# Kernel optimization log

Measured on AMD Instinct MI355X. Metric: run time of the kernel, lower is better.

Reference implementation:

```python
import jax, jax.numpy as jnp
import numpy as np

IN_F = 4096
OUT_F = 4096
N_TOK = 8192
MAX_ITER = IN_F * OUT_F // 2  # default max_iter=-1 -> half of weight entries


def _approx_matmul(x, weight, max_iter):
    """Budgeted approximate matmul: only the `max_iter` largest-magnitude
    weight entries participate (the rest of the multiply-accumulate budget is
    skipped). Faithful to the iteration-budget semantics of Approx_Matmul:
    max_iter multiply-adds out of in_features*out_features total.
    """
    n = weight.size
    flat_abs = jnp.abs(weight).reshape(-1)
    # threshold = k-th largest magnitude (static k -> jit-friendly)
    kth = jnp.sort(flat_abs)[n - max_iter]
    mask = (jnp.abs(weight) >= kth).astype(weight.dtype)
    w_eff = weight * jax.lax.stop_gradient(mask)
    # y[t, o] = sum_i x[t, i] * w_eff[o, i]
    return jnp.einsum('ti,oi->to', x, w_eff)


def setup_inputs() -> dict:
    key = jax.random.key(0)
    kx, kw, kb = jax.random.split(key, 3)
    x = jax.random.normal(kx, (N_TOK, IN_F), dtype=jnp.float32)
    # kaiming_uniform_(a=sqrt(5)) on [out, in] -> bound = 1/sqrt(in_features)
    bound = 1.0 / np.sqrt(IN_F)
    weight = jax.random.uniform(kw, (OUT_F, IN_F), dtype=jnp.float32,
                                minval=-bound, maxval=bound)
    bias = jax.random.uniform(kb, (OUT_F,), dtype=jnp.float32,
                              minval=-bound, maxval=bound)
    return {"x": x, "weight": weight, "bias": bias}


def reference(x, weight, bias):
    mid = _approx_matmul(x, weight, MAX_ITER)
    return mid + bias
```

## Files before the change

kernel.cpp:

```cpp
#include <hip/hip_runtime.h>

#define IN_F   4096
#define OUT_F  4096
#define N_TOK  8192
#define NW     (OUT_F * IN_F)
#define SEL_TARGET 8388608u
#define CAND_CAP (1u << 20)

#define LO_BITS 0x3BFCA000u
#define HI_BITS 0x3C018000u

typedef unsigned int  u32;
typedef unsigned short u16;

typedef __bf16 bf16x8 __attribute__((ext_vector_type(8)));
typedef float  f32x4  __attribute__((ext_vector_type(4)));

__device__ inline u16 f2bf_rne(float f) {
    u32 u = __float_as_uint(f);
    u32 r = (u + 0x7fffu + ((u >> 16) & 1u)) >> 16;
    return (u16)r;
}

__global__ __launch_bounds__(256) void scan1_kernel(const uint4* __restrict__ wb,
                                                    u32* __restrict__ cand,
                                                    u32* __restrict__ scal) {
    __shared__ u32 lbuf[4096];
    __shared__ u32 lcnt, gbase, lblw;
    if (threadIdx.x == 0) { lcnt = 0; lblw = 0; }
    __syncthreads();

    const int base = blockIdx.x * 4096;
    u32 cntb = 0;
    #pragma unroll 4
    for (int j = 0; j < 16; j++) {
        uint4 v = wb[base + threadIdx.x + j * 256];
        u32 k[4] = {v.x & 0x7fffffffu, v.y & 0x7fffffffu,
                    v.z & 0x7fffffffu, v.w & 0x7fffffffu};
        #pragma unroll
        for (int e = 0; e < 4; e++) {
            u32 kk = k[e];
            cntb += (kk < LO_BITS) ? 1u : 0u;
            if (kk >= LO_BITS && kk < HI_BITS) {
                u32 idx = atomicAdd(&lcnt, 1u);
                if (idx < 4096) lbuf[idx] = kk;
                else scal[6] = 1u;
            }
        }
    }
    #pragma unroll
    for (int off = 32; off; off >>= 1) cntb += __shfl_down(cntb, off);
    if ((threadIdx.x & 63) == 0) atomicAdd(&lblw, cntb);
    __syncthreads();
    if (threadIdx.x == 0) {
        gbase = atomicAdd(&scal[3], min(lcnt, 4096u));
        atomicAdd(&scal[4], lblw);
    }
    __syncthreads();
    const u32 n = min(lcnt, 4096u), gb = gbase;
    for (u32 i = threadIdx.x; i < n; i += 256)
        if (gb + i < CAND_CAP) cand[gb + i] = lbuf[i];
}

#define SCAN1024(part, t)                                            \
    do { _Pragma("unroll")                                           \
        for (int off_ = 1; off_ < 1024; off_ <<= 1) {                \
            u32 v_ = ((t) >= off_) ? part[(t) - off_] : 0u;          \
            __syncthreads();                                         \
            part[t] += v_;                                           \
            __syncthreads();                                         \
        } } while (0)

__global__ __launch_bounds__(1024) void select_win_kernel(const u32* __restrict__ cand,
                                                          const uint4* __restrict__ wb,
                                                          u32* __restrict__ scal) {
    __shared__ u32 h[2048];
    __shared__ u32 part[1024];
    __shared__ u32 sh[2];
    const int t = threadIdx.x;
    const u32 n = scal[3], below = scal[4], ovf = scal[6];
    const bool valid = (n > 0) && (n <= CAND_CAP) && (ovf == 0) &&
                       (below <= SEL_TARGET) && (SEL_TARGET < below + n);

    if (valid) {
        u32 tgt = SEL_TARGET - below;
        const uint4* c4 = (const uint4*)cand;
        const u32 n4 = n >> 2;

        h[t] = 0; h[t + 1024] = 0;
        __syncthreads();
        for (u32 i = t; i < n4; i += 1024) {
            uint4 v = c4[i];
            atomicAdd(&h[(v.x - LO_BITS) >> 9], 1u);
            atomicAdd(&h[(v.y - LO_BITS) >> 9], 1u);
            atomicAdd(&h[(v.z - LO_BITS) >> 9], 1u);
            atomicAdd(&h[(v.w - LO_BITS) >> 9], 1u);
        }
        for (u32 i = (n4 << 2) + t; i < n; i += 1024)
            atomicAdd(&h[(cand[i] - LO_BITS) >> 9], 1u);
        __syncthreads();
        u32 c = h[t];
        part[t] = c;
        __syncthreads();
        SCAN1024(part, t);
        u32 cum = (t == 0) ? 0u : part[t - 1];
        if (tgt >= cum && tgt < cum + c) { sh[0] = (u32)t; sh[1] = tgt - cum; }
        __syncthreads();
        const u32 b1 = sh[0];
        tgt = sh[1];
        __syncthreads();

        h[t] = 0; h[t + 1024] = 0;
        __syncthreads();
        for (u32 i = t; i < n4; i += 1024) {
            uint4 v = c4[i];
            u32 d0 = v.x - LO_BITS, d1 = v.y - LO_BITS,
                d2 = v.z - LO_BITS, d3 = v.w - LO_BITS;
            if ((d0 >> 9) == b1) atomicAdd(&h[d0 & 511u], 1u);
            if ((d1 >> 9) == b1) atomicAdd(&h[d1 & 511u], 1u);
            if ((d2 >> 9) == b1) atomicAdd(&h[d2 & 511u], 1u);
            if ((d3 >> 9) == b1) atomicAdd(&h[d3 & 511u], 1u);
        }
        for (u32 i = (n4 << 2) + t; i < n; i += 1024) {
            u32 d = cand[i] - LO_BITS;
            if ((d >> 9) == b1) atomicAdd(&h[d & 511u], 1u);
        }
        __syncthreads();
        c = (t < 512) ? h[t] : 0u;
        part[t] = c;
        __syncthreads();
        SCAN1024(part, t);
        cum = (t == 0) ? 0u : part[t - 1];
        if (tgt >= cum && tgt < cum + c)
            scal[2] = LO_BITS + (b1 << 9) + (u32)t;
        return;
    }

    u32 tgt = SEL_TARGET;
    const int nvec = NW / 4;
    h[t] = 0; h[t + 1024] = 0;
    __syncthreads();
    for (int i = t; i < nvec; i += 1024) {
        uint4 v = wb[i];
        atomicAdd(&h[(v.x & 0x7fffffffu) >> 20], 1u);
        atomicAdd(&h[(v.y & 0x7fffffffu) >> 20], 1u);
        atomicAdd(&h[(v.z & 0x7fffffffu) >> 20], 1u);
        atomicAdd(&h[(v.w & 0x7fffffffu) >> 20], 1u);
    }
    __syncthreads();
    u32 a0 = h[2 * t], a1 = h[2 * t + 1];
    part[t] = a0 + a1;
    __syncthreads();
    SCAN1024(part, t);
    u32 cum = (t == 0) ? 0u : part[t - 1];
    if (tgt >= cum && tgt < cum + a0) { sh[0] = (u32)(2 * t);     sh[1] = tgt - cum; }
    cum += a0;
    if (tgt >= cum && tgt < cum + a1) { sh[0] = (u32)(2 * t + 1); sh[1] = tgt - cum; }
    __syncthreads();
    const u32 b1f = sh[0];
    tgt = sh[1];
    __syncthreads();

    h[t] = 0; h[t + 1024] = 0;
    __syncthreads();
    for (int i = t; i < nvec; i += 1024) {
        uint4 v = wb[i];
        u32 k[4] = {v.x & 0x7fffffffu, v.y & 0x7fffffffu,
                    v.z & 0x7fffffffu, v.w & 0x7fffffffu};
        #pragma unroll
        for (int e = 0; e < 4; e++)
            if ((k[e] >> 20) == b1f) atomicAdd(&h[(k[e] >> 9) & 2047u], 1u);
    }
    __syncthreads();
    a0 = h[2 * t]; a1 = h[2 * t + 1];
    part[t] = a0 + a1;
    __syncthreads();
    SCAN1024(part, t);
    cum = (t == 0) ? 0u : part[t - 1];
    if (tgt >= cum && tgt < cum + a0) { sh[0] = (u32)(2 * t);     sh[1] = tgt - cum; }
    cum += a0;
    if (tgt >= cum && tgt < cum + a1) { sh[0] = (u32)(2 * t + 1); sh[1] = tgt - cum; }
    __syncthreads();
    const u32 pfx22 = (b1f << 11) | sh[0];
    tgt = sh[1];
    __syncthreads();

    h[t] = 0; h[t + 1024] = 0;
    __syncthreads();
    for (int i = t; i < nvec; i += 1024) {
        uint4 v = wb[i];
        u32 k[4] = {v.x & 0x7fffffffu, v.y & 0x7fffffffu,
                    v.z & 0x7fffffffu, v.w & 0x7fffffffu};
        #pragma unroll
        for (int e = 0; e < 4; e++)
            if ((k[e] >> 9) == pfx22) atomicAdd(&h[k[e] & 511u], 1u);
    }
    __syncthreads();
    u32 c = (t < 512) ? h[t] : 0u;
    part[t] = c;
    __syncthreads();
    SCAN1024(part, t);
    cum = (t == 0) ? 0u : part[t - 1];
    if (tgt >= cum && tgt < cum + c)
        scal[2] = (pfx22 << 9) | (u32)t;
}

__global__ __launch_bounds__(256) void convert_fused_kernel(
    const uint4* __restrict__ wb, const float4* __restrict__ xb,
    u16* __restrict__ w16, u16* __restrict__ x16,
    const u32* __restrict__ scal) {
    if (blockIdx.x < 1024) {
        const u32 kth = scal[2];
        const int stride = 1024 * 256;
        for (int i = blockIdx.x * 256 + threadIdx.x; i < NW / 4; i += stride) {
            uint4 v = wb[i];
            ushort4 o;
            o.x = ((v.x & 0x7fffffffu) >= kth) ? f2bf_rne(__uint_as_float(v.x)) : (u16)0;
            o.y = ((v.y & 0x7fffffffu) >= kth) ? f2bf_rne(__uint_as_float(v.y)) : (u16)0;
            o.z = ((v.z & 0x7fffffffu) >= kth) ? f2bf_rne(__uint_as_float(v.z)) : (u16)0;
            o.w = ((v.w & 0x7fffffffu) >= kth) ? f2bf_rne(__uint_as_float(v.w)) : (u16)0;
            *(ushort4*)&w16[(size_t)i * 4] = o;
        }
    } else {
        const int stride = 2048 * 256;
        for (int i = (blockIdx.x - 1024) * 256 + threadIdx.x;
             i < (N_TOK * IN_F) / 4; i += stride) {
            float4 v = xb[i];
            ushort4 o;
            o.x = f2bf_rne(v.x);
            o.y = f2bf_rne(v.y);
            o.z = f2bf_rne(v.z);
            o.w = f2bf_rne(v.w);
            *(ushort4*)&x16[(size_t)i * 4] = o;
        }
    }
}

#define BK 64
#define NT (IN_F / BK)

#define ASLOT(buf, ks) (((buf) * 2 + (ks)) * 8192)
#define BSLOT(buf, ks) (32768 + ((buf) * 2 + (ks)) * 8192)

#define VMCNT(n) asm volatile("s_waitcnt vmcnt(" #n ")" ::: "memory")
#define LGKM0    asm volatile("s_waitcnt lgkmcnt(0)" ::: "memory")
#define BARR()   __builtin_amdgcn_s_barrier()

__global__ __launch_bounds__(512, 2) void gemm8p(
    const u16* __restrict__ A,
    const u16* __restrict__ B,
    const float* __restrict__ bias,
    float* __restrict__ C) {
    __shared__ u16 lds[65536];

    const int tid  = threadIdx.x;
    const int lane = tid & 63;
    const int ln15 = lane & 15;
    const int l16  = lane >> 4;
    const int wv   = tid >> 6;
    const int wr   = wv >> 2;
    const int wc   = wv & 3;
    const int wrow = wr * 128;
    const int wcol = wc * 64;

    const int bid = blockIdx.x;
    const int swz = (bid & 7) * 64 + (bid >> 3);
    const int by  = swz >> 4;
    const int bx  = swz & 15;
    const int arow = by * 256;
    const int brow = bx * 256;

    f32x4 acc[8][4];
    #pragma unroll
    for (int m = 0; m < 8; m++)
        #pragma unroll
        for (int n = 0; n < 4; n++)
            acc[m][n] = {0.f, 0.f, 0.f, 0.f};

    #define STAGE(G, rowbase, kt, ks, slot) do {                                        \
        _Pragma("unroll")                                                               \
        for (int i_ = 0; i_ < 2; i_++) {                                                \
            int q_  = tid + i_ * 512;                                                   \
            int r_  = q_ >> 2;                                                          \
            int cs_ = (q_ & 3) ^ ((r_ >> 1) & 3);                                       \
            const u16* src_ = (G) + (size_t)((rowbase) + r_) * IN_F                     \
                              + (kt) * BK + (ks) * 32 + cs_ * 8;                        \
            __builtin_amdgcn_global_load_lds(                                           \
                (const __attribute__((address_space(1))) unsigned int*)src_,            \
                (__attribute__((address_space(3))) unsigned int*)&lds[(slot) + q_ * 8], \
                16, 0, 0);                                                              \
        } } while (0)

    #define READ_A(mh, ks, buf) do {                                                    \
        _Pragma("unroll")                                                               \
        for (int i_ = 0; i_ < 4; i_++) {                                                \
            int row_ = wrow + ((mh) * 4 + i_) * 16 + ln15;                              \
            int cc_  = l16 ^ ((row_ >> 1) & 3);                                         \
            aF[i_] = *(const bf16x8*)&lds[ASLOT(buf, ks) + row_ * 32 + cc_ * 8];        \
        } } while (0)

    #define READ_B(ks, buf) do {                                                       \
        _Pragma("unroll")                                                               \
        for (int i_ = 0; i_ < 4; i_++) {                                                \
            int row_ = wcol + i_ * 16 + ln15;                                           \
            int cc_  = l16 ^ ((row_ >> 1) & 3);                                         \
            bF[i_] = *(const bf16x8*)&lds[BSLOT(buf, ks) + row_ * 32 + cc_ * 8];        \
        } } while (0)

    #define MFMAQ(mh) do {                                                              \
        __builtin_amdgcn_s_setprio(1);                                                  \
        _Pragma("unroll")                                                               \
        for (int i_ = 0; i_ < 4; i_++)                                                  \
            _Pragma("unroll")                                                           \
            for (int n_ = 0; n_ < 4; n_++)                                              \
                acc[(mh) * 4 + i_][n_] = __builtin_amdgcn_mfma_f32_16x16x32_bf16(       \
                    aF[i_], bF[n_], acc[(mh) * 4 + i_][n_], 0, 0, 0);                   \
        __builtin_amdgcn_s_setprio(0);                                                  \
    } while (0)

    STAGE(B, brow, 0, 0, BSLOT(0, 0));
    STAGE(A, arow, 0, 0, ASLOT(0, 0));
    STAGE(B, brow, 0, 1, BSLOT(0, 1));
    STAGE(A, arow, 0, 1, ASLOT(0, 1));
    VMCNT(4);
    STAGE(B, brow, 1, 0, BSLOT(1, 0));
    STAGE(A, arow, 1, 0, ASLOT(1, 0));
    STAGE(B, brow, 1, 1, BSLOT(1, 1));
    VMCNT(6);
    BARR();

    bf16x8 aF[4], bF[4];

    #pragma unroll 1
    for (int it = 0; it < NT / 2; it++) {
        const int t0 = 2 * it;
        const int ka = t0 + 1;
        const int kb = (t0 + 2 < NT) ? t0 + 2 : NT - 1;
        const int kc = (t0 + 3 < NT) ? t0 + 3 : NT - 1;

        READ_A(0, 0, 0); READ_B(0, 0);
        STAGE(A, arow, ka, 1, ASLOT(1, 1));
        BARR(); LGKM0; MFMAQ(0); BARR();
        READ_A(1, 0, 0);
        STAGE(B, brow, kb, 0, BSLOT(0, 0));
        BARR(); LGKM0; MFMAQ(1); BARR();
        READ_A(0, 1, 0); READ_B(1, 0);
        STAGE(A, arow, kb, 0, ASLOT(0, 0));
        BARR(); LGKM0; MFMAQ(0); BARR();
        READ_A(1, 1, 0);
        STAGE(B, brow, kb, 1, BSLOT(0, 1));
        VMCNT(6);
        BARR(); LGKM0; MFMAQ(1); BARR();

        READ_A(0, 0, 1); READ_B(0, 1);
        STAGE(A, arow, kb, 1, ASLOT(0, 1));
        BARR(); LGKM0; MFMAQ(0); BARR();
        READ_A(1, 0, 1);
        STAGE(B, brow, kc, 0, BSLOT(1, 0));
        BARR(); LGKM0; MFMAQ(1); BARR();
        READ_A(0, 1, 1); READ_B(1, 1);
        STAGE(A, arow, kc, 0, ASLOT(1, 0));
        BARR(); LGKM0; MFMAQ(0); BARR();
        READ_A(1, 1, 1);
        STAGE(B, brow, kc, 1, BSLOT(1, 1));
        VMCNT(6);
        BARR(); LGKM0; MFMAQ(1); BARR();
    }
    VMCNT(0);

    const int cr = l16 * 4;
    #pragma unroll
    for (int n = 0; n < 4; n++) {
        int col = brow + wcol + n * 16 + ln15;
        float bv = bias[col];
        #pragma unroll
        for (int m = 0; m < 8; m++) {
            int r0 = arow + wrow + m * 16 + cr;
            #pragma unroll
            for (int j = 0; j < 4; j++) {
                C[(size_t)(r0 + j) * OUT_F + col] = acc[m][n][j] + bv;
            }
        }
    }
}

extern "C" void kernel_launch(void* const* d_in, const int* in_sizes, int n_in,
                              void* d_out, int out_size, void* d_ws, size_t ws_size,
                              hipStream_t stream) {
    const float* x    = (const float*)d_in[0];
    const float* w    = (const float*)d_in[1];
    const float* bias = (const float*)d_in[2];
    float* out = (float*)d_out;

    char* ws = (char*)d_ws;
    u32* scal  = (u32*)(ws + 0);
    u16* w16   = (u16*)(ws + 65536);
    u16* x16   = (u16*)(ws + 65536 + (size_t)NW * 2);
    u32* cand  = (u32*)((char*)x16 + 131072);

    hipMemsetAsync(scal, 0, 64, stream);

    scan1_kernel<<<1024, 256, 0, stream>>>((const uint4*)w, cand, scal);
    select_win_kernel<<<1, 1024, 0, stream>>>(cand, (const uint4*)w, scal);

    convert_fused_kernel<<<3072, 256, 0, stream>>>((const uint4*)w, (const float4*)x,
                                                   w16, x16, scal);

    gemm8p<<<512, 512, 0, stream>>>(x16, w16, bias, out);
}
```

Measured before the change: 366.8 us.

## Fuse x conversion into scan kernel and use nontemporal loads/stores

Moves the x fp32-to-bf16 conversion out of the post-select conversion kernel and into the first scan kernel, so it runs alongside the weight candidate scan. The weight conversion becomes its own kernel with 2048 blocks. Nontemporal loads are added for the streaming reads and nontemporal stores for the GEMM output, and the candidate buffer now aliases the w16 workspace. The aliasing relies on select finishing before convert_w overwrites that memory, which stream ordering guarantees.

```diff
diff --git a/kernel.cpp b/kernel.cpp
--- a/kernel.cpp
+++ b/kernel.cpp
@@ -15,6 +15,7 @@
 
 typedef __bf16 bf16x8 __attribute__((ext_vector_type(8)));
 typedef float  f32x4  __attribute__((ext_vector_type(4)));
+typedef u32    u32x4  __attribute__((ext_vector_type(4)));
 
 __device__ inline u16 f2bf_rne(float f) {
     u32 u = __float_as_uint(f);
@@ -22,44 +23,59 @@
     return (u16)r;
 }
 
-__global__ __launch_bounds__(256) void scan1_kernel(const uint4* __restrict__ wb,
-                                                    u32* __restrict__ cand,
-                                                    u32* __restrict__ scal) {
-    __shared__ u32 lbuf[4096];
-    __shared__ u32 lcnt, gbase, lblw;
-    if (threadIdx.x == 0) { lcnt = 0; lblw = 0; }
-    __syncthreads();
-
-    const int base = blockIdx.x * 4096;
-    u32 cntb = 0;
-    #pragma unroll 4
-    for (int j = 0; j < 16; j++) {
-        uint4 v = wb[base + threadIdx.x + j * 256];
-        u32 k[4] = {v.x & 0x7fffffffu, v.y & 0x7fffffffu,
-                    v.z & 0x7fffffffu, v.w & 0x7fffffffu};
+__global__ __launch_bounds__(256) void front_fused_kernel(
+    const uint4* __restrict__ wb, const f32x4* __restrict__ xb,
+    u32* __restrict__ cand, u16* __restrict__ x16,
+    u32* __restrict__ scal) {
+    if (blockIdx.x < 1024) {
+        __shared__ u32 lbuf[4096];
+        __shared__ u32 lcnt, gbase, lblw;
+        if (threadIdx.x == 0) { lcnt = 0; lblw = 0; }
+        __syncthreads();
+
+        const int base = blockIdx.x * 4096;
+        u32 cntb = 0;
+        #pragma unroll 4
+        for (int j = 0; j < 16; j++) {
+            uint4 v = wb[base + threadIdx.x + j * 256];
+            u32 k[4] = {v.x & 0x7fffffffu, v.y & 0x7fffffffu,
+                        v.z & 0x7fffffffu, v.w & 0x7fffffffu};
+            #pragma unroll
+            for (int e = 0; e < 4; e++) {
+                u32 kk = k[e];
+                cntb += (kk < LO_BITS) ? 1u : 0u;
+                if (kk >= LO_BITS && kk < HI_BITS) {
+                    u32 idx = atomicAdd(&lcnt, 1u);
+                    if (idx < 4096) lbuf[idx] = kk;
+                    else scal[6] = 1u;
+                }
+            }
+        }
         #pragma unroll
-        for (int e = 0; e < 4; e++) {
-            u32 kk = k[e];
-            cntb += (kk < LO_BITS) ? 1u : 0u;
-            if (kk >= LO_BITS && kk < HI_BITS) {
-                u32 idx = atomicAdd(&lcnt, 1u);
-                if (idx < 4096) lbuf[idx] = kk;
-                else scal[6] = 1u;
-            }
-        }
-    }
-    #pragma unroll
-    for (int off = 32; off; off >>= 1) cntb += __shfl_down(cntb, off);
-    if ((threadIdx.x & 63) == 0) atomicAdd(&lblw, cntb);
-    __syncthreads();
-    if (threadIdx.x == 0) {
-        gbase = atomicAdd(&scal[3], min(lcnt, 4096u));
-        atomicAdd(&scal[4], lblw);
-    }
-    __syncthreads();
-    const u32 n = min(lcnt, 4096u), gb = gbase;
-    for (u32 i = threadIdx.x; i < n; i += 256)
-        if (gb + i < CAND_CAP) cand[gb + i] = lbuf[i];
+        for (int off = 32; off; off >>= 1) cntb += __shfl_down(cntb, off);
+        if ((threadIdx.x & 63) == 0) atomicAdd(&lblw, cntb);
+        __syncthreads();
+        if (threadIdx.x == 0) {
+            gbase = atomicAdd(&scal[3], min(lcnt, 4096u));
+            atomicAdd(&scal[4], lblw);
+        }
+        __syncthreads();
+        const u32 n = min(lcnt, 4096u), gb = gbase;
+        for (u32 i = threadIdx.x; i < n; i += 256)
+            if (gb + i < CAND_CAP) cand[gb + i] = lbuf[i];
+    } else {
+        const int stride = 2048 * 256;
+        for (int i = (blockIdx.x - 1024) * 256 + threadIdx.x;
+             i < (N_TOK * IN_F) / 4; i += stride) {
+            f32x4 v = __builtin_nontemporal_load(&xb[i]);
+            ushort4 o;
+            o.x = f2bf_rne(v.x);
+            o.y = f2bf_rne(v.y);
+            o.z = f2bf_rne(v.z);
+            o.w = f2bf_rne(v.w);
+            *(ushort4*)&x16[(size_t)i * 4] = o;
+        }
+    }
 }
 
 #define SCAN1024(part, t)                                            \
@@ -205,34 +221,20 @@
         scal[2] = (pfx22 << 9) | (u32)t;
 }
 
-__global__ __launch_bounds__(256) void convert_fused_kernel(
-    const uint4* __restrict__ wb, const float4* __restrict__ xb,
-    u16* __restrict__ w16, u16* __restrict__ x16,
-    const u32* __restrict__ scal) {
-    if (blockIdx.x < 1024) {
-        const u32 kth = scal[2];
-        const int stride = 1024 * 256;
-        for (int i = blockIdx.x * 256 + threadIdx.x; i < NW / 4; i += stride) {
-            uint4 v = wb[i];
-            ushort4 o;
-            o.x = ((v.x & 0x7fffffffu) >= kth) ? f2bf_rne(__uint_as_float(v.x)) : (u16)0;
-            o.y = ((v.y & 0x7fffffffu) >= kth) ? f2bf_rne(__uint_as_float(v.y)) : (u16)0;
-            o.z = ((v.z & 0x7fffffffu) >= kth) ? f2bf_rne(__uint_as_float(v.z)) : (u16)0;
-            o.w = ((v.w & 0x7fffffffu) >= kth) ? f2bf_rne(__uint_as_float(v.w)) : (u16)0;
-            *(ushort4*)&w16[(size_t)i * 4] = o;
-        }
-    } else {
-        const int stride = 2048 * 256;
-        for (int i = (blockIdx.x - 1024) * 256 + threadIdx.x;
-             i < (N_TOK * IN_F) / 4; i += stride) {
-            float4 v = xb[i];
-            ushort4 o;
-            o.x = f2bf_rne(v.x);
-            o.y = f2bf_rne(v.y);
-            o.z = f2bf_rne(v.z);
-            o.w = f2bf_rne(v.w);
-            *(ushort4*)&x16[(size_t)i * 4] = o;
-        }
+__global__ __launch_bounds__(256) void convert_w_kernel(const u32x4* __restrict__ wb,
+                                                        u16* __restrict__ w16,
+                                                        const u32* __restrict__ scal) {
+    const u32 kth = scal[2];
+    const int nvec = NW / 4;
+    const int stride = gridDim.x * blockDim.x;
+    for (int i = blockIdx.x * blockDim.x + threadIdx.x; i < nvec; i += stride) {
+        u32x4 v = __builtin_nontemporal_load(&wb[i]);
+        ushort4 o;
+        o.x = ((v.x & 0x7fffffffu) >= kth) ? f2bf_rne(__uint_as_float(v.x)) : (u16)0;
+        o.y = ((v.y & 0x7fffffffu) >= kth) ? f2bf_rne(__uint_as_float(v.y)) : (u16)0;
+        o.z = ((v.z & 0x7fffffffu) >= kth) ? f2bf_rne(__uint_as_float(v.z)) : (u16)0;
+        o.w = ((v.w & 0x7fffffffu) >= kth) ? f2bf_rne(__uint_as_float(v.w)) : (u16)0;
+        *(ushort4*)&w16[(size_t)i * 4] = o;
     }
 }
 
@@ -378,7 +380,8 @@
             int r0 = arow + wrow + m * 16 + cr;
             #pragma unroll
             for (int j = 0; j < 4; j++) {
-                C[(size_t)(r0 + j) * OUT_F + col] = acc[m][n][j] + bv;
+                float vv = acc[m][n][j] + bv;
+                __builtin_nontemporal_store(vv, &C[(size_t)(r0 + j) * OUT_F + col]);
             }
         }
     }
@@ -396,15 +399,14 @@
     u32* scal  = (u32*)(ws + 0);
     u16* w16   = (u16*)(ws + 65536);
     u16* x16   = (u16*)(ws + 65536 + (size_t)NW * 2);
-    u32* cand  = (u32*)((char*)x16 + 131072);
+    u32* cand  = (u32*)w16;
 
     hipMemsetAsync(scal, 0, 64, stream);
 
-    scan1_kernel<<<1024, 256, 0, stream>>>((const uint4*)w, cand, scal);
+    front_fused_kernel<<<3072, 256, 0, stream>>>((const uint4*)w, (const f32x4*)x,
+                                                 cand, x16, scal);
     select_win_kernel<<<1, 1024, 0, stream>>>(cand, (const uint4*)w, scal);
-
-    convert_fused_kernel<<<3072, 256, 0, stream>>>((const uint4*)w, (const float4*)x,
-                                                   w16, x16, scal);
+    convert_w_kernel<<<2048, 256, 0, stream>>>((const u32x4*)w, w16, scal);
 
     gemm8p<<<512, 512, 0, stream>>>(x16, w16, bias, out);
 }
```

New measurement: 347.6 us. -5.2%, faster.
